# Kernel tuning notes

Measured on AMD Instinct MI355X. Metric: run time of the kernel, lower is better.

Reference implementation:

```python
import jax, jax.numpy as jnp
import numpy as np

K = 15  # kNN neighbors, matches init kwarg


def _knn_edges(x, k):
    # brute-force kNN, flow='target_to_source': row = center node, col = neighbor
    sq = jnp.sum(x * x, axis=-1)
    d2 = sq[:, None] - 2.0 * (x @ x.T) + sq[None, :]          # [N,N]
    n = x.shape[0]
    d2 = jnp.where(jnp.eye(n, dtype=bool), jnp.inf, d2)        # exclude self-loops
    _, idx = jax.lax.top_k(-d2, k)                             # [N,k] nearest
    row = jnp.repeat(jnp.arange(n), k)
    col = idx.reshape(-1)
    return jnp.stack([row, col])                               # [2, N*k]


def _scatter_softmax(a, seg, n):
    m = jax.ops.segment_max(a, seg, num_segments=n)
    m = jnp.where(jnp.isfinite(m), m, 0.0)
    e = jnp.exp(a - m[seg])
    s = jax.ops.segment_sum(e, seg, num_segments=n)
    return e / s[seg]


def _devconv(x, edges, W_theta, b_theta, W_phi, b_phi):
    # DevConv (neural mesh simplification): W_phi . max_{j in N(i)} W_theta(x_i - x_j)
    row, col = edges[0], edges[1]
    h = (x[row] - x[col]) @ W_theta.T + b_theta                # [E, H]
    agg = jax.ops.segment_max(h, row, num_segments=x.shape[0])  # [N, H]
    agg = jnp.where(jnp.isfinite(agg), agg, 0.0)               # guard empty rows
    return agg @ W_phi.T + b_phi


def setup_inputs() -> dict:
    key = jax.random.key(0)
    ks = jax.random.split(key, 8)
    N, E, H, C = 4096, 65536, 64, 3
    x = jax.random.normal(ks[0], (N, C), dtype=jnp.float32)
    edge_index = jax.random.randint(ks[1], (2, E), 0, N, dtype=jnp.int64)
    s_in, s_h = 1.0 / np.sqrt(C), 1.0 / np.sqrt(H)
    return {
        "x": x,
        "edge_index": edge_index,
        "W_theta": jax.random.normal(ks[2], (H, C), dtype=jnp.float32) * s_in,
        "b_theta": jnp.zeros((H,), dtype=jnp.float32),
        "W_phi": jax.random.normal(ks[3], (H, H), dtype=jnp.float32) * s_h,
        "b_phi": jnp.zeros((H,), dtype=jnp.float32),
        "W_q": jax.random.normal(ks[4], (H, H), dtype=jnp.float32) * s_h,
        "W_k": jax.random.normal(ks[5], (H, H), dtype=jnp.float32) * s_h,
    }


def reference(x, edge_index, W_theta, b_theta, W_phi, b_phi, W_q, W_k):
    n = x.shape[0]
    knn = _knn_edges(x, K)
    extended = jnp.concatenate([edge_index, knn], axis=1)
    feats = _devconv(x, extended, W_theta, b_theta, W_phi, b_phi)  # [N, H]
    row, col = edge_index[0], edge_index[1]
    q = feats @ W_q.T
    kf = feats @ W_k.T
    attn = jnp.sum(q[row] * kf[col], axis=-1)                  # [E]
    scores = _scatter_softmax(attn, row, n)                     # [E]
    # S, A as dense NxN (duplicates summed, matching sparse coalescing)
    S = jnp.zeros((n, n), dtype=x.dtype).at[row, col].add(scores)
    A = jnp.zeros((n, n), dtype=x.dtype).at[row, col].add(1.0)
    A_s = S @ A @ S.T                                           # simplified adjacency
    return A_s
```

## Files before the change

kernel.cpp:

```cpp
#include <hip/hip_runtime.h>
#include <math.h>

#define HN 64
#define KNN 15

__device__ __forceinline__ unsigned fenc(float f){
  unsigned u = __float_as_uint(f);
  return (u & 0x80000000u) ? ~u : (u | 0x80000000u);
}

__device__ __forceinline__ unsigned long long u64min(unsigned long long a, unsigned long long b){
  return a < b ? a : b;
}
__device__ __forceinline__ unsigned long long shfl_xor_u64(unsigned long long v, int mask){
  unsigned lo = (unsigned)v, hi = (unsigned)(v >> 32);
  lo = __shfl_xor((int)lo, mask, 64);
  hi = __shfl_xor((int)hi, mask, 64);
  return ((unsigned long long)hi << 32) | lo;
}

__device__ __forceinline__ void edge_load(const void* ei, int E, int n, int e, int& r, int& c){
  const long long* L = (const long long*)ei;
  long long vr = L[e];
  bool ok = (vr >= 0 && vr < (long long)n);
  unsigned long long bal = __ballot(ok);
  unsigned long long act = __ballot(true);
  if (bal == act){
    r = (int)vr;
    c = (int)L[E + e];
  } else {
    const int* I = (const int*)ei;
    r = I[e];
    c = I[E + e];
  }
}

__global__ void __launch_bounds__(256) k_mega(
    const float* __restrict__ x, const float* __restrict__ Wt, const void* ei,
    float* __restrict__ y, int* __restrict__ knn_cols,
    int* __restrict__ cnt, int* __restrict__ ccnt,
    int N, int E, int nbY, int nbC){
  __shared__ unsigned denc[4096];
  __shared__ unsigned long long mk[256];
  int b = blockIdx.x, t = threadIdx.x;
  if (b < nbY){
    int gid = b * 256 + t;
    if (gid < N * HN){
      int nn = gid >> 6, h = gid & 63;
      y[gid] = x[nn*3] * Wt[h*3] + x[nn*3+1] * Wt[h*3+1] + x[nn*3+2] * Wt[h*3+2];
    }
    return;
  }
  if (b < nbY + nbC){
    int e = (b - nbY) * 256 + t;
    if (e < E){
      int r, c;
      edge_load(ei, E, N, e, r, c);
      atomicAdd(&cnt[r], 1);
      atomicAdd(&ccnt[c], 1);
    }
    return;
  }
  int i = b - nbY - nbC;
  float xi0 = x[i*3], xi1 = x[i*3+1], xi2 = x[i*3+2];
  float sqi = xi0*xi0 + xi1*xi1 + xi2*xi2;
  unsigned long long best = ~0ULL;
  #pragma unroll
  for (int m = 0; m < 16; ++m){
    int j = t + 256*m;
    float a = x[j*3], bb = x[j*3+1], c = x[j*3+2];
    float sqj = a*a + bb*bb + c*c;
    float dot = xi0*a + xi1*bb + xi2*c;
    float d2 = (sqi - 2.0f*dot) + sqj;
    unsigned e = (j == i) ? 0xFFFFFFFFu : fenc(d2);
    denc[j] = e;
    best = u64min(best, ((unsigned long long)e << 32) | (unsigned)j);
  }
  mk[t] = best;
  __syncthreads();
  if (t >= 64) return;
  unsigned long long k0 = mk[t], k1 = mk[t+64], k2 = mk[t+128], k3 = mk[t+192];
  for (int m = 0; m < KNN; ++m){
    unsigned long long mm = u64min(u64min(k0, k1), u64min(k2, k3));
    #pragma unroll
    for (int off = 1; off < 64; off <<= 1)
      mm = u64min(mm, shfl_xor_u64(mm, off));
    int j = (int)(mm & 0xFFFFFFFFu);
    if (t == 0) knn_cols[i*KNN + m] = j;
    if ((j & 63) == t){
      int slot = j & 255;
      denc[j] = 0xFFFFFFFFu;
      unsigned long long nb = ~0ULL;
      #pragma unroll
      for (int m2 = 0; m2 < 16; ++m2){
        int jj = slot + 256*m2;
        nb = u64min(nb, ((unsigned long long)denc[jj] << 32) | (unsigned)jj);
      }
      int kreg = (j >> 6) & 3;
      if (kreg == 0) k0 = nb; else if (kreg == 1) k1 = nb;
      else if (kreg == 2) k2 = nb; else k3 = nb;
    }
  }
}

__global__ void k_scan2(const int* __restrict__ cnt, int* __restrict__ ptr,
                        const int* __restrict__ ccnt, int* __restrict__ cptr, int n){
  __shared__ int part[1024];
  const int* src = (blockIdx.x == 0) ? cnt : ccnt;
  int* dst = (blockIdx.x == 0) ? ptr : cptr;
  int t = threadIdx.x;
  int base = t * 4;
  int a0 = src[base], a1 = src[base+1], a2 = src[base+2], a3 = src[base+3];
  int s = a0 + a1 + a2 + a3;
  part[t] = s;
  __syncthreads();
  for (int off = 1; off < 1024; off <<= 1){
    int v = (t >= off) ? part[t - off] : 0;
    __syncthreads();
    part[t] += v;
    __syncthreads();
  }
  int excl = part[t] - s;
  dst[base]   = excl;
  dst[base+1] = excl + a0;
  dst[base+2] = excl + a0 + a1;
  dst[base+3] = excl + a0 + a1 + a2;
  if (t == 1023) dst[n] = part[1023];
}

__global__ void k_fill(const void* ei, const int* __restrict__ ptr,
                       int* __restrict__ fillo, const int* __restrict__ cnt,
                       const int* __restrict__ knncols, int* __restrict__ ecol,
                       int N, int E, int nbE){
  int b = blockIdx.x, t = threadIdx.x;
  if (b < nbE){
    int e = b * 256 + t;
    if (e < E){
      int r, c;
      edge_load(ei, E, N, e, r, c);
      int pos = ptr[r] + KNN*r + atomicAdd(&fillo[r], 1);
      ecol[pos] = c;
    }
  } else {
    int gid = (b - nbE) * 256 + t;
    if (gid < N * KNN){
      int i = gid / KNN, m = gid - i * KNN;
      ecol[ptr[i] + KNN*i + cnt[i] + m] = knncols[gid];
    }
  }
}

__global__ void k_dev(const int* __restrict__ ptr, const int* __restrict__ ecol,
                      const float* __restrict__ y, const float* __restrict__ bt,
                      const float* __restrict__ Wp, const float* __restrict__ bp,
                      const float* __restrict__ Wq, const float* __restrict__ Wk,
                      float* __restrict__ q, float* __restrict__ kf, int n){
  __shared__ float sag[256];
  __shared__ float sft[256];
  int t = threadIdx.x;
  int i = blockIdx.x * 4 + (t >> 6);
  int h = t & 63;
  int beg = ptr[i] + KNN*i;
  int end = ptr[i+1] + KNN*(i+1);
  float m = INFINITY;
  for (int idx = beg; idx < end; ++idx)
    m = fminf(m, y[ecol[idx]*HN + h]);
  sag[t] = y[i*HN + h] + bt[h] - m;
  __syncthreads();
  int nn = t >> 6;
  float acc = bp[h];
  #pragma unroll 8
  for (int c = 0; c < HN; ++c) acc += sag[nn*HN + c] * Wp[h*HN + c];
  sft[t] = acc;
  __syncthreads();
  float aq = 0.f, ak = 0.f;
  #pragma unroll 8
  for (int c = 0; c < HN; ++c){
    float f = sft[nn*HN + c];
    aq += f * Wq[h*HN + c];
    ak += f * Wk[h*HN + c];
  }
  size_t o = (size_t)blockIdx.x * 256 + t;
  q[o] = aq;
  kf[o] = ak;
}

__global__ void __launch_bounds__(256) k_rowattn(
    const int* __restrict__ ptr, const int* __restrict__ cptr,
    const int* __restrict__ ecol, const float* __restrict__ q,
    const float* __restrict__ kf, float* __restrict__ sval,
    int2* __restrict__ csp, int* __restrict__ cfill, int n){
  int t = threadIdx.x;
  int lane = t & 63;
  int r = blockIdx.x * 4 + (t >> 6);
  if (r >= n) return;
  int base = ptr[r];
  int deg = ptr[r+1] - base;
  if (deg == 0) return;
  int ebase = base + KNN*r;
  float qh = q[(size_t)r*HN + lane];
  float mx = -INFINITY;
  for (int s = 0; s < deg; ++s){
    int c = ecol[ebase + s];
    float part = qh * kf[(size_t)c*HN + lane];
    #pragma unroll
    for (int off = 1; off < 64; off <<= 1) part += __shfl_xor(part, off, 64);
    if (lane == 0) sval[base + s] = part;
    mx = fmaxf(mx, part);
  }
  float lsum = 0.f;
  for (int s = lane; s < deg; s += 64){
    float e = expf(sval[base + s] - mx);
    sval[base + s] = e;
    lsum += e;
  }
  #pragma unroll
  for (int off = 1; off < 64; off <<= 1) lsum += __shfl_xor(lsum, off, 64);
  for (int s = lane; s < deg; s += 64){
    float v = sval[base + s] / lsum;
    sval[base + s] = v;
    int c = ecol[ebase + s];
    int pos = cptr[c] + atomicAdd(&cfill[c], 1);
    csp[pos] = make_int2(r, __float_as_int(v));
  }
}

__global__ void __launch_bounds__(256) k_prod(
    const int* __restrict__ ptr, const int* __restrict__ cnt,
    const int* __restrict__ ecol, const float* __restrict__ sval,
    const int* __restrict__ cptr, const int2* __restrict__ csp,
    float* __restrict__ out, int n){
  __shared__ float orow[4096];
  int t = threadIdx.x;
  int lane = t & 63;
  int w = t >> 6;
  int i = blockIdx.x;
  float4 z = {0.f, 0.f, 0.f, 0.f};
  float4* o4 = (float4*)orow;
  #pragma unroll
  for (int ch = 0; ch < 4; ++ch) o4[ch*256 + t] = z;
  __syncthreads();
  int base = ptr[i];
  int len = ptr[i+1] - base;
  int ebase = base + KNN*i;
  int qs = lane >> 2, rq = lane & 3;
  for (int p = w; p < len; p += 4){
    int k = ecol[ebase + p];
    float v = sval[base + p];
    int kbase = ptr[k];
    int klen = ptr[k+1] - kbase;
    int kebase = kbase + KNN*k;
    for (int qq = qs; qq < klen; qq += 16){
      int l = ecol[kebase + qq];
      int rb = cptr[l], re = cptr[l+1];
      for (int rr = rb + rq; rr < re; rr += 4){
        int2 e2 = csp[rr];
        atomicAdd(&orow[e2.x], v * __int_as_float(e2.y));
      }
    }
  }
  __syncthreads();
  float4* dst = (float4*)(out + (size_t)i * n);
  #pragma unroll
  for (int ch = 0; ch < 4; ++ch) dst[ch*256 + t] = o4[ch*256 + t];
}

extern "C" void kernel_launch(void* const* d_in, const int* in_sizes, int n_in,
                              void* d_out, int out_size, void* d_ws, size_t ws_size,
                              hipStream_t stream) {
  const float* x   = (const float*)d_in[0];
  const void*  ei  = d_in[1];
  const float* Wt  = (const float*)d_in[2];
  const float* bt  = (const float*)d_in[3];
  const float* Wp  = (const float*)d_in[4];
  const float* bp  = (const float*)d_in[5];
  const float* Wq  = (const float*)d_in[6];
  const float* Wk  = (const float*)d_in[7];
  float* out = (float*)d_out;

  const int N = in_sizes[0] / 3;
  const int E = in_sizes[1] / 2;

  char* p = (char*)d_ws;
  auto alloc = [&](size_t bytes) -> void* {
    void* r = (void*)p;
    p += (bytes + 255) & ~(size_t)255;
    return r;
  };
  int*      ctr     = (int*)  alloc((size_t)4*N*4);
  int*      cnt     = ctr;
  int*      ccnt    = ctr + N;
  int*      cfill   = ctr + 2*N;
  int*      fillo   = ctr + 3*N;

  float*    y       = (float*)alloc((size_t)N*HN*4);
  float*    q       = (float*)alloc((size_t)N*HN*4);
  float*    kf      = (float*)alloc((size_t)N*HN*4);
  int*      ptrb    = (int*)  alloc((size_t)(N+1)*4);
  int*      cptrb   = (int*)  alloc((size_t)(N+1)*4);
  int*      ecol    = (int*)  alloc((size_t)(E + N*KNN)*4);
  float*    sval    = (float*)alloc((size_t)E*4);
  int2*     csp     = (int2*) alloc((size_t)E*8);
  int*      knncols = (int*)  alloc((size_t)N*KNN*4);

  hipMemsetAsync(ctr, 0, (size_t)4*N*4, stream);

  int nbY = (N*HN + 255)/256;
  int nbC = (E + 255)/256;
  int nbK = (N*KNN + 255)/256;

  k_mega<<<nbY + nbC + N, 256, 0, stream>>>(x, Wt, ei, y, knncols, cnt, ccnt,
                                            N, E, nbY, nbC);
  k_scan2<<<2, 1024, 0, stream>>>(cnt, ptrb, ccnt, cptrb, N);
  k_fill<<<nbC + nbK, 256, 0, stream>>>(ei, ptrb, fillo, cnt, knncols, ecol,
                                        N, E, nbC);
  k_dev<<<N/4, 256, 0, stream>>>(ptrb, ecol, y, bt, Wp, bp, Wq, Wk, q, kf, N);
  k_rowattn<<<N/4, 256, 0, stream>>>(ptrb, cptrb, ecol, q, kf, sval, csp, cfill, N);
  k_prod<<<N, 256, 0, stream>>>(ptrb, cnt, ecol, sval, cptrb, csp, out, N);
}
```

Before: 297.3 us.

## Pack row/col offsets and scores into int2 records, lane-parallel attention dots

The scan kernel now also writes packed (offset, count) records for rows and columns. Attention writes packed (col, score) pairs so the product kernel fetches fewer dependent scalars per hop. In the attention kernel each lane computes a whole dot product with float4 loads instead of doing a 64-lane shuffle reduction per edge. The product kernel handles two output rows per 512-thread block. The aim is to shorten dependent-load chains in the irregular sparse triple product, at the cost of extra workspace and higher register and LDS use.

```diff
diff --git a/kernel.cpp b/kernel.cpp
--- a/kernel.cpp
+++ b/kernel.cpp
@@ -104,7 +104,8 @@
 }
 
 __global__ void k_scan2(const int* __restrict__ cnt, int* __restrict__ ptr,
-                        const int* __restrict__ ccnt, int* __restrict__ cptr, int n){
+                        const int* __restrict__ ccnt, int* __restrict__ cptr,
+                        int2* __restrict__ rinfo, int2* __restrict__ cinfo, int n){
   __shared__ int part[1024];
   const int* src = (blockIdx.x == 0) ? cnt : ccnt;
   int* dst = (blockIdx.x == 0) ? ptr : cptr;
@@ -121,11 +122,23 @@
     __syncthreads();
   }
   int excl = part[t] - s;
-  dst[base]   = excl;
-  dst[base+1] = excl + a0;
-  dst[base+2] = excl + a0 + a1;
-  dst[base+3] = excl + a0 + a1 + a2;
+  int v0 = excl, v1 = excl + a0, v2 = excl + a0 + a1, v3 = excl + a0 + a1 + a2;
+  dst[base]   = v0;
+  dst[base+1] = v1;
+  dst[base+2] = v2;
+  dst[base+3] = v3;
   if (t == 1023) dst[n] = part[1023];
+  if (blockIdx.x == 0){
+    rinfo[base]   = make_int2(v0 + KNN*base,     a0);
+    rinfo[base+1] = make_int2(v1 + KNN*(base+1), a1);
+    rinfo[base+2] = make_int2(v2 + KNN*(base+2), a2);
+    rinfo[base+3] = make_int2(v3 + KNN*(base+3), a3);
+  } else {
+    cinfo[base]   = make_int2(v0, a0);
+    cinfo[base+1] = make_int2(v1, a1);
+    cinfo[base+2] = make_int2(v2, a2);
+    cinfo[base+3] = make_int2(v3, a3);
+  }
 }
 
 __global__ void k_fill(const void* ei, const int* __restrict__ ptr,
@@ -186,10 +199,11 @@
 }
 
 __global__ void __launch_bounds__(256) k_rowattn(
-    const int* __restrict__ ptr, const int* __restrict__ cptr,
+    const int* __restrict__ ptr, const int2* __restrict__ cinfo,
     const int* __restrict__ ecol, const float* __restrict__ q,
     const float* __restrict__ kf, float* __restrict__ sval,
-    int2* __restrict__ csp, int* __restrict__ cfill, int n){
+    int2* __restrict__ scp, int2* __restrict__ csp,
+    int* __restrict__ cfill, int n){
   int t = threadIdx.x;
   int lane = t & 63;
   int r = blockIdx.x * 4 + (t >> 6);
@@ -198,16 +212,25 @@
   int deg = ptr[r+1] - base;
   if (deg == 0) return;
   int ebase = base + KNN*r;
-  float qh = q[(size_t)r*HN + lane];
+  float4 qv[16];
+  const float4* qr = (const float4*)(q + (size_t)r*HN);
+  #pragma unroll
+  for (int m = 0; m < 16; ++m) qv[m] = qr[m];
   float mx = -INFINITY;
-  for (int s = 0; s < deg; ++s){
+  for (int s = lane; s < deg; s += 64){
     int c = ecol[ebase + s];
-    float part = qh * kf[(size_t)c*HN + lane];
+    const float4* kc = (const float4*)(kf + (size_t)c*HN);
+    float acc = 0.f;
     #pragma unroll
-    for (int off = 1; off < 64; off <<= 1) part += __shfl_xor(part, off, 64);
-    if (lane == 0) sval[base + s] = part;
-    mx = fmaxf(mx, part);
-  }
+    for (int m = 0; m < 16; ++m){
+      float4 b = kc[m];
+      acc += qv[m].x*b.x + qv[m].y*b.y + qv[m].z*b.z + qv[m].w*b.w;
+    }
+    sval[base + s] = acc;
+    mx = fmaxf(mx, acc);
+  }
+  #pragma unroll
+  for (int off = 1; off < 64; off <<= 1) mx = fmaxf(mx, __shfl_xor(mx, off, 64));
   float lsum = 0.f;
   for (int s = lane; s < deg; s += 64){
     float e = expf(sval[base + s] - mx);
@@ -218,51 +241,51 @@
   for (int off = 1; off < 64; off <<= 1) lsum += __shfl_xor(lsum, off, 64);
   for (int s = lane; s < deg; s += 64){
     float v = sval[base + s] / lsum;
-    sval[base + s] = v;
     int c = ecol[ebase + s];
-    int pos = cptr[c] + atomicAdd(&cfill[c], 1);
+    scp[base + s] = make_int2(c, __float_as_int(v));
+    int pos = cinfo[c].x + atomicAdd(&cfill[c], 1);
     csp[pos] = make_int2(r, __float_as_int(v));
   }
 }
 
-__global__ void __launch_bounds__(256) k_prod(
-    const int* __restrict__ ptr, const int* __restrict__ cnt,
-    const int* __restrict__ ecol, const float* __restrict__ sval,
-    const int* __restrict__ cptr, const int2* __restrict__ csp,
+__global__ void __launch_bounds__(512) k_prod(
+    const int* __restrict__ ptr, const int2* __restrict__ scp,
+    const int2* __restrict__ rinfo, const int* __restrict__ ecol,
+    const int2* __restrict__ cinfo, const int2* __restrict__ csp,
     float* __restrict__ out, int n){
-  __shared__ float orow[4096];
+  __shared__ float orow[2][4096];
   int t = threadIdx.x;
+  int half = t >> 8;
+  int tt = t & 255;
   int lane = t & 63;
-  int w = t >> 6;
-  int i = blockIdx.x;
+  int w = (t >> 6) & 3;
+  int i = blockIdx.x * 2 + half;
   float4 z = {0.f, 0.f, 0.f, 0.f};
-  float4* o4 = (float4*)orow;
-  #pragma unroll
-  for (int ch = 0; ch < 4; ++ch) o4[ch*256 + t] = z;
+  float4* o4 = (float4*)orow[half];
+  #pragma unroll
+  for (int ch = 0; ch < 4; ++ch) o4[ch*256 + tt] = z;
   __syncthreads();
   int base = ptr[i];
   int len = ptr[i+1] - base;
-  int ebase = base + KNN*i;
   int qs = lane >> 2, rq = lane & 3;
+  float* my = orow[half];
   for (int p = w; p < len; p += 4){
-    int k = ecol[ebase + p];
-    float v = sval[base + p];
-    int kbase = ptr[k];
-    int klen = ptr[k+1] - kbase;
-    int kebase = kbase + KNN*k;
-    for (int qq = qs; qq < klen; qq += 16){
-      int l = ecol[kebase + qq];
-      int rb = cptr[l], re = cptr[l+1];
-      for (int rr = rb + rq; rr < re; rr += 4){
-        int2 e2 = csp[rr];
-        atomicAdd(&orow[e2.x], v * __int_as_float(e2.y));
+    int2 kv = scp[base + p];
+    float v = __int_as_float(kv.y);
+    int2 ri = rinfo[kv.x];
+    for (int qq = qs; qq < ri.y; qq += 16){
+      int l = ecol[ri.x + qq];
+      int2 ci = cinfo[l];
+      for (int rr = rq; rr < ci.y; rr += 4){
+        int2 e2 = csp[ci.x + rr];
+        atomicAdd(&my[e2.x], v * __int_as_float(e2.y));
       }
     }
   }
   __syncthreads();
   float4* dst = (float4*)(out + (size_t)i * n);
   #pragma unroll
-  for (int ch = 0; ch < 4; ++ch) dst[ch*256 + t] = o4[ch*256 + t];
+  for (int ch = 0; ch < 4; ++ch) dst[ch*256 + tt] = o4[ch*256 + tt];
 }
 
 extern "C" void kernel_launch(void* const* d_in, const int* in_sizes, int n_in,
@@ -298,8 +321,11 @@
   float*    kf      = (float*)alloc((size_t)N*HN*4);
   int*      ptrb    = (int*)  alloc((size_t)(N+1)*4);
   int*      cptrb   = (int*)  alloc((size_t)(N+1)*4);
+  int2*     rinfo   = (int2*) alloc((size_t)N*8);
+  int2*     cinfo   = (int2*) alloc((size_t)N*8);
   int*      ecol    = (int*)  alloc((size_t)(E + N*KNN)*4);
   float*    sval    = (float*)alloc((size_t)E*4);
+  int2*     scp     = (int2*) alloc((size_t)E*8);
   int2*     csp     = (int2*) alloc((size_t)E*8);
   int*      knncols = (int*)  alloc((size_t)N*KNN*4);
 
@@ -311,10 +337,11 @@
 
   k_mega<<<nbY + nbC + N, 256, 0, stream>>>(x, Wt, ei, y, knncols, cnt, ccnt,
                                             N, E, nbY, nbC);
-  k_scan2<<<2, 1024, 0, stream>>>(cnt, ptrb, ccnt, cptrb, N);
+  k_scan2<<<2, 1024, 0, stream>>>(cnt, ptrb, ccnt, cptrb, rinfo, cinfo, N);
   k_fill<<<nbC + nbK, 256, 0, stream>>>(ei, ptrb, fillo, cnt, knncols, ecol,
                                         N, E, nbC);
   k_dev<<<N/4, 256, 0, stream>>>(ptrb, ecol, y, bt, Wp, bp, Wq, Wk, q, kf, N);
-  k_rowattn<<<N/4, 256, 0, stream>>>(ptrb, cptrb, ecol, q, kf, sval, csp, cfill, N);
-  k_prod<<<N, 256, 0, stream>>>(ptrb, cnt, ecol, sval, cptrb, csp, out, N);
-}
+  k_rowattn<<<N/4, 256, 0, stream>>>(ptrb, cinfo, ecol, q, kf, sval, scp, csp,
+                                     cfill, N);
+  k_prod<<<N/2, 512, 0, stream>>>(ptrb, scp, rinfo, ecol, cinfo, csp, out, N);
+}
```

After: 291.3 us. 2.0% less time.
